# Performance work log

Hardware: AMD Instinct MI355X
Metric: run time of the kernel (lower is better)

## Reference

```python
import jax, jax.numpy as jnp
import numpy as np

EPS = 1e-5
B, S, D = 4, 2048, 128
BALL_SCALE = 0.05  # keeps points inside the unit Poincare ball for c=1


def setup_inputs() -> dict:
    key = jax.random.key(0)
    kq, kk, kv = jax.random.split(key, 3)
    q = jax.random.normal(kq, (B, S, D), dtype=jnp.float32) * BALL_SCALE
    k = jax.random.normal(kk, (B, S, D), dtype=jnp.float32) * BALL_SCALE
    v_tangent = jax.random.normal(kv, (B, S, D), dtype=jnp.float32)
    c = jnp.asarray(1.0, dtype=jnp.float32)
    beta = jnp.asarray(0.0, dtype=jnp.float32)            # nn.Parameter init 0.0
    attention_bias = jnp.asarray(0.0, dtype=jnp.float32)  # nn.Parameter init 0.0
    return {"q": q, "k": k, "v_tangent": v_tangent, "c": c,
            "beta": beta, "attention_bias": attention_bias}


def reference(q, k, v_tangent, c, beta, attention_bias):
    sqrt_c = jnp.sqrt(c)

    # --- pairwise Poincare distance (all fp32, as in the torch autocast block) ---
    x_norm_sq = jnp.sum(q * q, axis=-1, keepdims=True)            # (B,S,1)
    y_norm_sq = jnp.sum(k * k, axis=-1, keepdims=True)            # (B,S,1)
    xy_dot = jnp.einsum('bsd,btd->bst', q, k)                     # (B,S,S)
    y_norm_sq_t = jnp.swapaxes(y_norm_sq, -2, -1)                 # (B,1,S)
    diff_norm_sq = x_norm_sq - 2.0 * xy_dot + y_norm_sq_t         # ||x-y||^2, (B,S,S)
    denom = (1.0 - c * x_norm_sq) * (1.0 - c * y_norm_sq_t)       # (B,S,S)
    arg = 1.0 + 2.0 * c * diff_norm_sq / jnp.maximum(denom, EPS)
    dist = jnp.arccosh(jnp.maximum(arg, 1.0 + EPS)) / sqrt_c      # (B,S,S)

    # --- attention ---
    beta_positive = jax.nn.softplus(beta)
    attention_scores = -beta_positive * dist - attention_bias
    attention_weights = jax.nn.softmax(attention_scores, axis=-1)  # (B,S,S)
    output_tangent = jnp.einsum('bst,btd->bsd', attention_weights, v_tangent)

    # --- exp map at origin ---
    v_norm = jnp.maximum(
        jnp.sqrt(jnp.sum(output_tangent * output_tangent, axis=-1, keepdims=True)), EPS)
    output_hyperbolic = (jnp.tanh(sqrt_c * v_norm) / sqrt_c) * (output_tangent / v_norm)

    return output_hyperbolic, attention_weights
```

## Files before the change

### kernel.cpp

```cpp
#include <hip/hip_runtime.h>
#include <math.h>

#define B_ 4
#define S_ 2048
#define D_ 128
#define EPSF 1e-5f
#define BN 128
#define PSB 272

typedef __attribute__((ext_vector_type(8))) short short8;
typedef __attribute__((ext_vector_type(4))) float f32x4;

static __device__ __forceinline__ unsigned short f2bf(float f) {
    unsigned u = __float_as_uint(f);
    return (unsigned short)((u + 0x7fffu + ((u >> 16) & 1u)) >> 16);
}

static __device__ __forceinline__ void gload_lds16(const void* g, void* l) {
    __builtin_amdgcn_global_load_lds((const __attribute__((address_space(1))) unsigned*)g,
                                     (__attribute__((address_space(3))) unsigned*)l, 16, 0, 0);
}


__global__ __launch_bounds__(256) void convqk_kernel(const float* __restrict__ q,
                                                     const float* __restrict__ k,
                                                     float* __restrict__ qn, float* __restrict__ kn,
                                                     float* __restrict__ lws,
                                                     unsigned* __restrict__ Qb, unsigned* __restrict__ Kb) {
    int row = blockIdx.x * 4 + (threadIdx.x >> 6);
    int lane = threadIdx.x & 63;
    const int NR = B_ * S_;
    bool isQ = row < NR;
    int r = isQ ? row : row - NR;
    float2 v = ((const float2*)(isQ ? q : k))[(size_t)r * 64 + lane];
    unsigned pk = (unsigned)f2bf(v.x) | ((unsigned)f2bf(v.y) << 16);
    float nrm = v.x * v.x + v.y * v.y;
#pragma unroll
    for (int m = 1; m <= 32; m <<= 1) nrm += __shfl_xor(nrm, m, 64);
    if (isQ) {
        Qb[(size_t)r * 64 + lane] = pk;
        if (lane == 0) qn[r] = nrm;
        if (lane == 1) lws[r] = 0.f;
    } else {
        int c = lane >> 2;
        int cs = c ^ (r & 7);
        Kb[(size_t)r * 64 + cs * 4 + (lane & 3)] = pk;
        if (lane == 0) kn[r] = nrm;
    }
}

__global__ __launch_bounds__(256) void convv_kernel(const float* __restrict__ v, uint4* __restrict__ Vtb) {
    __shared__ unsigned short Vs[128 * 132];
    int b = blockIdx.x >> 4;
    int t = blockIdx.x & 15;
    int tid = threadIdx.x;
    const float* src = v + ((size_t)b * S_ + t * 128) * D_;
    int d4 = tid & 31, key0 = tid >> 5;
#pragma unroll
    for (int it = 0; it < 16; ++it) {
        int key = key0 + it * 8;
        float4 f = *(const float4*)(src + (size_t)key * D_ + d4 * 4);
        unsigned short* dst = &Vs[key * 132 + d4 * 4];
        dst[0] = f2bf(f.x); dst[1] = f2bf(f.y); dst[2] = f2bf(f.z); dst[3] = f2bf(f.w);
    }
    __syncthreads();
    uint4* tile = Vtb + (size_t)blockIdx.x * (128 * 16);
    int d = tid & 127;
    int cl = tid >> 7;
#pragma unroll
    for (int it = 0; it < 8; ++it) {
        int c = cl + it * 2;
        int kb = c * 8;
        unsigned short e0 = Vs[(kb + 0) * 132 + d], e1 = Vs[(kb + 1) * 132 + d];
        unsigned short e2 = Vs[(kb + 2) * 132 + d], e3 = Vs[(kb + 3) * 132 + d];
        unsigned short e4 = Vs[(kb + 4) * 132 + d], e5 = Vs[(kb + 5) * 132 + d];
        unsigned short e6 = Vs[(kb + 6) * 132 + d], e7 = Vs[(kb + 7) * 132 + d];
        uint4 o;
        o.x = (unsigned)e0 | ((unsigned)e1 << 16);
        o.y = (unsigned)e2 | ((unsigned)e3 << 16);
        o.z = (unsigned)e4 | ((unsigned)e5 << 16);
        o.w = (unsigned)e6 | ((unsigned)e7 << 16);
        tile[d * 16 + (c ^ (d & 7))] = o;
    }
}


__global__ __launch_bounds__(512, 2) void hattn2_kernel(
    const unsigned short* __restrict__ Qb, const char* __restrict__ Kb, const char* __restrict__ Vtb,
    const float* __restrict__ qn, const float* __restrict__ kn,
    const float* __restrict__ cp, const float* __restrict__ betap, const float* __restrict__ biasp,
    float* __restrict__ lws, float* __restrict__ Opart, uint4* __restrict__ Pws) {

    __shared__ __align__(1024) char smem[76032];
    char* KsB = smem;
    char* VtB = smem + 32768;
    char* PsB = smem + 65536;
    float* yn_s  = (float*)(smem + 74240);
    float* gy_s  = (float*)(smem + 74752);
    float* xn_s  = (float*)(smem + 75264);
    float* rx_s  = (float*)(smem + 75392);
    float* l_row = (float*)(smem + 75520);

    const int tid = threadIdx.x;
    const int lane = tid & 63, wave = tid >> 6;
    const int wm = wave & 1, wn = wave >> 1;
    const int lm = lane & 15, quad = lane >> 4;

    const int th = blockIdx.x & 1;
    const int b = (blockIdx.x >> 1) & 3;
    const int rb = blockIdx.x >> 3;
    const int s0 = rb * 32;
    const size_t bS = (size_t)b * S_;

    const float cc = cp[0], beta = betap[0], bias = biasp[0];
    const float beta_pos = fmaxf(beta, 0.f) + log1pf(__expf(-fabsf(beta)));
    const float sqrt_c = sqrtf(cc);
    const float bneg = -beta_pos / sqrt_c;
    const float bias2 = -bias * 1.442695040888963f;
    const float onepe = 1.f + EPSF;
    const float c2 = 2.f * cc;

    if (tid < 32) {
        float xn = qn[bS + s0 + tid];
        xn_s[tid] = xn;
        rx_s[tid] = c2 * __builtin_amdgcn_rcpf(1.f - cc * xn);
        l_row[tid] = 0.f;
    }

    short8 aq[4];
    {
        const unsigned short* qrow = Qb + (bS + s0 + wm * 16 + lm) * D_;
#pragma unroll
        for (int ks = 0; ks < 4; ++ks)
            aq[ks] = *(const short8*)(qrow + ks * 32 + quad * 8);
    }

    f32x4 o0 = {0.f, 0.f, 0.f, 0.f}, o1 = {0.f, 0.f, 0.f, 0.f};

    const char* KbBase = Kb + bS * 256;
    const char* VtBase = Vtb + (size_t)b * 16 * 32768;

    for (int it = 0; it < 8; ++it) {
        int t = th * 8 + it;
        int t0 = t * BN;
        __syncthreads();
        {
            const char* ks = KbBase + (size_t)t0 * 256;
            const char* vs = VtBase + (size_t)t * 32768;
#pragma unroll
            for (int j = 0; j < 4; ++j) {
                int off = (tid + j * 512) * 16;
                gload_lds16(ks + off, KsB + off);
                gload_lds16(vs + off, VtB + off);
            }
            if (tid < BN) {
                float yn = kn[bS + t0 + tid];
                yn_s[tid] = yn;
                gy_s[tid] = __builtin_amdgcn_rcpf(1.f - cc * yn);
            }
        }
        __syncthreads();

        f32x4 acc0 = {0.f, 0.f, 0.f, 0.f}, acc1 = {0.f, 0.f, 0.f, 0.f};
#pragma unroll
        for (int ks = 0; ks < 4; ++ks) {
            int n0 = wn * 32 + lm;
            int c = ks * 4 + quad;
            short8 b0 = *(const short8*)(KsB + n0 * 256 + ((c ^ (n0 & 7)) * 16));
            int n1 = n0 + 16;
            short8 b1 = *(const short8*)(KsB + n1 * 256 + ((c ^ (n1 & 7)) * 16));
            acc0 = __builtin_amdgcn_mfma_f32_16x16x32_bf16(aq[ks], b0, acc0, 0, 0, 0);
            acc1 = __builtin_amdgcn_mfma_f32_16x16x32_bf16(aq[ks], b1, acc1, 0, 0, 0);
        }

        int col0 = wn * 32 + lm, col1 = col0 + 16;
        float yn0 = yn_s[col0], gy0 = gy_s[col0];
        float yn1 = yn_s[col1], gy1 = gy_s[col1];
#pragma unroll
        for (int r = 0; r < 4; ++r) {
            int row = wm * 16 + quad * 4 + r;
            float xn = xn_s[row];
            float rx = rx_s[row];

            float diff0 = fmaf(-2.f, acc0[r], xn + yn0);
            float arg0 = fmaf(diff0 * gy0, rx, 1.f);
            arg0 = fmaxf(arg0, onepe);
            float w0 = arg0 + sqrtf(fmaf(arg0, arg0, -1.f));
            float p0 = __builtin_amdgcn_exp2f(fmaf(bneg, __builtin_amdgcn_logf(w0), bias2));

            float diff1 = fmaf(-2.f, acc1[r], xn + yn1);
            float arg1 = fmaf(diff1 * gy1, rx, 1.f);
            arg1 = fmaxf(arg1, onepe);
            float w1 = arg1 + sqrtf(fmaf(arg1, arg1, -1.f));
            float p1 = __builtin_amdgcn_exp2f(fmaf(bneg, __builtin_amdgcn_logf(w1), bias2));

            *(unsigned short*)(PsB + row * PSB + col0 * 2) = f2bf(p0);
            *(unsigned short*)(PsB + row * PSB + col1 * 2) = f2bf(p1);

            float s = p0 + p1;
#pragma unroll
            for (int m = 1; m <= 8; m <<= 1) s += __shfl_xor(s, m, 64);
            if (lm == 0) atomicAdd(&l_row[row], s);
        }
        __syncthreads();

        {
            int row = tid >> 4, chunk = tid & 15;
            uint4 pv = *(const uint4*)(PsB + row * PSB + chunk * 16);
            Pws[(((bS + s0 + row) * S_ + t0) >> 3) + chunk] = pv;
        }

#pragma unroll
        for (int ks = 0; ks < 4; ++ks) {
            short8 ap = *(const short8*)(PsB + (wm * 16 + lm) * PSB + (ks * 32 + quad * 8) * 2);
            int d0 = wn * 32 + lm;
            int c = ks * 4 + quad;
            short8 v0 = *(const short8*)(VtB + d0 * 256 + ((c ^ (d0 & 7)) * 16));
            int d1 = d0 + 16;
            short8 v1 = *(const short8*)(VtB + d1 * 256 + ((c ^ (d1 & 7)) * 16));
            o0 = __builtin_amdgcn_mfma_f32_16x16x32_bf16(ap, v0, o0, 0, 0, 0);
            o1 = __builtin_amdgcn_mfma_f32_16x16x32_bf16(ap, v1, o1, 0, 0, 0);
        }
    }
    __syncthreads();

    float* op = Opart + (size_t)th * (B_ * S_ * D_) + (bS + s0) * D_;
#pragma unroll
    for (int r = 0; r < 4; ++r) {
        int row = wm * 16 + quad * 4 + r;
        op[(size_t)row * D_ + wn * 32 + lm] = o0[r];
        op[(size_t)row * D_ + wn * 32 + 16 + lm] = o1[r];
    }
    if (tid < 32) atomicAdd(&lws[bS + s0 + tid], l_row[tid]);
}

__global__ __launch_bounds__(256) void hepi_kernel(const float* __restrict__ Opart,
                                                   const float* __restrict__ lws,
                                                   const float* __restrict__ cp,
                                                   float* __restrict__ hout) {
    int row = blockIdx.x * 4 + (threadIdx.x >> 6);
    int lane = threadIdx.x & 63;
    const float cc = cp[0];
    const float sqrt_c = sqrtf(cc);
    float2 a = ((const float2*)(Opart + (size_t)row * D_))[lane];
    float2 b = ((const float2*)(Opart + (size_t)(B_ * S_ * D_) + (size_t)row * D_))[lane];
    float linv = 1.f / lws[row];
    float x0 = (a.x + b.x) * linv;
    float x1 = (a.y + b.y) * linv;
    float np = x0 * x0 + x1 * x1;
#pragma unroll
    for (int m = 1; m <= 32; m <<= 1) np += __shfl_xor(np, m, 64);
    float vn = fmaxf(sqrtf(np), EPSF);
    float aa = sqrt_c * vn;
    float t = 1.f - 2.f / (__expf(2.f * aa) + 1.f);
    float sc = t / aa;
    float2 o = {x0 * sc, x1 * sc};
    ((float2*)(hout + (size_t)row * D_))[lane] = o;
}

__global__ __launch_bounds__(256) void wnorm2_kernel(const uint4* __restrict__ Pws,
                                                     const float* __restrict__ lws,
                                                     float* __restrict__ w) {
    size_t idx = (size_t)blockIdx.x * 256 + threadIdx.x;
    int row = (int)(idx >> 8);
    float linv = 1.f / lws[row];
    uint4 u = Pws[idx];
    float4 f0, f1;
    f0.x = __uint_as_float(u.x << 16) * linv;
    f0.y = __uint_as_float(u.x & 0xffff0000u) * linv;
    f0.z = __uint_as_float(u.y << 16) * linv;
    f0.w = __uint_as_float(u.y & 0xffff0000u) * linv;
    f1.x = __uint_as_float(u.z << 16) * linv;
    f1.y = __uint_as_float(u.z & 0xffff0000u) * linv;
    f1.z = __uint_as_float(u.w << 16) * linv;
    f1.w = __uint_as_float(u.w & 0xffff0000u) * linv;
    float4* out = (float4*)w + idx * 2;
    out[0] = f0;
    out[1] = f1;
}


__global__ __launch_bounds__(512, 2) void hattn_kernel(
    const unsigned short* __restrict__ Qb, const char* __restrict__ Kb, const char* __restrict__ Vtb,
    const float* __restrict__ qn, const float* __restrict__ kn,
    const float* __restrict__ cp, const float* __restrict__ betap, const float* __restrict__ biasp,
    float* __restrict__ lws, float* __restrict__ houtg, float* __restrict__ woutg) {

    __shared__ __align__(1024) char smem[75136];
    char* KsB = smem;
    char* VtB = smem + 32768;
    char* PsB = smem + 65536;
    float* kn_s  = (float*)(smem + 74240);
    float* qn_s  = (float*)(smem + 74752);
    float* l_row = (float*)(smem + 74880);
    float* nsq_s = (float*)(smem + 75008);

    const int tid = threadIdx.x;
    const int lane = tid & 63, wave = tid >> 6;
    const int wm = wave & 1, wn = wave >> 1;
    const int lm = lane & 15, quad = lane >> 4;

    int xcd = blockIdx.x & 7;
    int b = xcd >> 1;
    int rb = (blockIdx.x >> 3) * 2 + (xcd & 1);
    int s0 = rb * 32;
    const size_t bS = (size_t)b * S_;

    const float cc = cp[0], beta = betap[0], bias = biasp[0];
    const float beta_pos = fmaxf(beta, 0.f) + log1pf(__expf(-fabsf(beta)));
    const float sqrt_c = sqrtf(cc);
    const float inv_sqrt_c = 1.f / sqrt_c;

    if (tid < 32) {
        qn_s[tid] = qn[bS + s0 + tid];
        l_row[tid] = 0.f;
        nsq_s[tid] = 0.f;
    }

    short8 aq[4];
    {
        const unsigned short* qrow = Qb + (bS + s0 + wm * 16 + lm) * D_;
#pragma unroll
        for (int ks = 0; ks < 4; ++ks)
            aq[ks] = *(const short8*)(qrow + ks * 32 + quad * 8);
    }

    f32x4 o0 = {0.f, 0.f, 0.f, 0.f}, o1 = {0.f, 0.f, 0.f, 0.f};

    const char* KbBase = Kb + bS * 256;
    const char* VtBase = Vtb + (size_t)b * 16 * 32768;

    for (int t = 0; t < S_ / BN; ++t) {
        int t0 = t * BN;
        __syncthreads();
        {
            const uint4* ksrc = (const uint4*)(KbBase + (size_t)t0 * 256);
            const uint4* vsrc = (const uint4*)(VtBase + (size_t)t * 32768);
            uint4* kd = (uint4*)KsB;
            uint4* vd = (uint4*)VtB;
#pragma unroll
            for (int i = 0; i < 4; ++i) {
                kd[tid + i * 512] = ksrc[tid + i * 512];
                vd[tid + i * 512] = vsrc[tid + i * 512];
            }
            if (tid < BN) kn_s[tid] = kn[bS + t0 + tid];
        }
        __syncthreads();

        f32x4 acc0 = {0.f, 0.f, 0.f, 0.f}, acc1 = {0.f, 0.f, 0.f, 0.f};
#pragma unroll
        for (int ks = 0; ks < 4; ++ks) {
            int n0 = wn * 32 + lm;
            int c = ks * 4 + quad;
            short8 b0 = *(const short8*)(KsB + n0 * 256 + ((c ^ (n0 & 7)) * 16));
            int n1 = n0 + 16;
            short8 b1 = *(const short8*)(KsB + n1 * 256 + ((c ^ (n1 & 7)) * 16));
            acc0 = __builtin_amdgcn_mfma_f32_16x16x32_bf16(aq[ks], b0, acc0, 0, 0, 0);
            acc1 = __builtin_amdgcn_mfma_f32_16x16x32_bf16(aq[ks], b1, acc1, 0, 0, 0);
        }

        float lp[4];
#pragma unroll
        for (int r = 0; r < 4; ++r) {
            int row = wm * 16 + quad * 4 + r;
            float xn = qn_s[row];
            float fx = 1.f - cc * xn;
            float p0, p1;
#pragma unroll
            for (int nt = 0; nt < 2; ++nt) {
                int col = wn * 32 + nt * 16 + lm;
                float dot = (nt == 0) ? acc0[r] : acc1[r];
                float yn = kn_s[col];
                float diff = xn - 2.f * dot + yn;
                float den = fmaxf(fx * (1.f - cc * yn), EPSF);
                float arg = fmaf(2.f * cc * diff, __builtin_amdgcn_rcpf(den), 1.f);
                arg = fmaxf(arg, 1.f + EPSF);
                float dist = __logf(arg + sqrtf(arg * arg - 1.f)) * inv_sqrt_c;
                float p = __expf(fmaf(-beta_pos, dist, -bias));
                woutg[(bS + s0 + row) * S_ + t0 + col] = p;
                *(unsigned short*)(PsB + row * PSB + col * 2) = f2bf(p);
                if (nt == 0) p0 = p; else p1 = p;
            }
            lp[r] = p0 + p1;
        }
#pragma unroll
        for (int r = 0; r < 4; ++r) {
            float s = lp[r];
#pragma unroll
            for (int m = 1; m <= 8; m <<= 1) s += __shfl_xor(s, m, 64);
            if (lm == 0) atomicAdd(&l_row[wm * 16 + quad * 4 + r], s);
        }
        __syncthreads();

#pragma unroll
        for (int ks = 0; ks < 4; ++ks) {
            short8 ap = *(const short8*)(PsB + (wm * 16 + lm) * PSB + (ks * 32 + quad * 8) * 2);
            int d0 = wn * 32 + lm;
            int c = ks * 4 + quad;
            short8 v0 = *(const short8*)(VtB + d0 * 256 + ((c ^ (d0 & 7)) * 16));
            int d1 = d0 + 16;
            short8 v1 = *(const short8*)(VtB + d1 * 256 + ((c ^ (d1 & 7)) * 16));
            o0 = __builtin_amdgcn_mfma_f32_16x16x32_bf16(ap, v0, o0, 0, 0, 0);
            o1 = __builtin_amdgcn_mfma_f32_16x16x32_bf16(ap, v1, o1, 0, 0, 0);
        }
    }
    __syncthreads();

    float xs0[4], xs1[4];
#pragma unroll
    for (int r = 0; r < 4; ++r) {
        int row = wm * 16 + quad * 4 + r;
        float linv = __builtin_amdgcn_rcpf(l_row[row]);
        float x0 = o0[r] * linv, x1 = o1[r] * linv;
        xs0[r] = x0; xs1[r] = x1;
        float np = x0 * x0 + x1 * x1;
#pragma unroll
        for (int m = 1; m <= 8; m <<= 1) np += __shfl_xor(np, m, 64);
        if (lm == 0) atomicAdd(&nsq_s[row], np);
    }
    if (tid < 32) lws[bS + s0 + tid] = l_row[tid];
    __syncthreads();
#pragma unroll
    for (int r = 0; r < 4; ++r) {
        int row = wm * 16 + quad * 4 + r;
        float vn = fmaxf(sqrtf(nsq_s[row]), EPSF);
        float a = sqrt_c * vn;
        float th = 1.f - 2.f * __builtin_amdgcn_rcpf(__expf(2.f * a) + 1.f);
        float sc = th / a;
        houtg[(bS + s0 + row) * D_ + wn * 32 + lm] = xs0[r] * sc;
        houtg[(bS + s0 + row) * D_ + wn * 32 + 16 + lm] = xs1[r] * sc;
    }
}

__global__ __launch_bounds__(256) void wnorm_kernel(float* __restrict__ w,
                                                    const float* __restrict__ lws) {
    size_t idx = (size_t)blockIdx.x * 256 + threadIdx.x;
    int row = (int)(idx >> 9);
    float linv = 1.f / lws[row];
    float4* p = (float4*)w + idx;
    float4 v = *p;
    v.x *= linv; v.y *= linv; v.z *= linv; v.w *= linv;
    *p = v;
}


extern "C" void kernel_launch(void* const* d_in, const int* in_sizes, int n_in,
                              void* d_out, int out_size, void* d_ws, size_t ws_size,
                              hipStream_t stream) {
    const float* q    = (const float*)d_in[0];
    const float* k    = (const float*)d_in[1];
    const float* v    = (const float*)d_in[2];
    const float* c    = (const float*)d_in[3];
    const float* beta = (const float*)d_in[4];
    const float* ab   = (const float*)d_in[5];

    float* out  = (float*)d_out;
    float* hout = out;
    float* wout = out + (size_t)B_ * S_ * D_;

    float* qn  = (float*)d_ws;
    float* kn  = qn + B_ * S_;
    float* lws = kn + B_ * S_;
    char*  wsb = (char*)d_ws;
    const size_t QB_OFF = 98304;
    const size_t KB_OFF = QB_OFF + 2097152;
    const size_t VT_OFF = KB_OFF + 2097152;
    const size_t NEED1  = VT_OFF + 2097152;
    const size_t OP_OFF = NEED1;
    const size_t PW_OFF = OP_OFF + 2u * B_ * S_ * D_ * 4;
    const size_t NEED2  = PW_OFF + (size_t)B_ * S_ * S_ * 2;

    unsigned* Qb = (unsigned*)(wsb + QB_OFF);
    unsigned* Kb = (unsigned*)(wsb + KB_OFF);
    uint4*   Vtb = (uint4*)(wsb + VT_OFF);

    if (ws_size >= NEED2) {
        float* Opart = (float*)(wsb + OP_OFF);
        uint4* Pws   = (uint4*)(wsb + PW_OFF);
        convqk_kernel<<<4096, 256, 0, stream>>>(q, k, qn, kn, lws, Qb, Kb);
        convv_kernel<<<64, 256, 0, stream>>>(v, Vtb);
        hattn2_kernel<<<512, 512, 0, stream>>>((const unsigned short*)Qb, (const char*)Kb,
                                               (const char*)Vtb, qn, kn, c, beta, ab,
                                               lws, Opart, Pws);
        hepi_kernel<<<2048, 256, 0, stream>>>(Opart, lws, c, hout);
        wnorm2_kernel<<<8192, 256, 0, stream>>>(Pws, lws, wout);
    } else {
        convqk_kernel<<<4096, 256, 0, stream>>>(q, k, qn, kn, lws, Qb, Kb);
        convv_kernel<<<64, 256, 0, stream>>>(v, Vtb);
        hattn_kernel<<<256, 512, 0, stream>>>((const unsigned short*)Qb, (const char*)Kb,
                                              (const char*)Vtb, qn, kn, c, beta, ab,
                                              lws, hout, wout);
        wnorm_kernel<<<(B_ * S_ * S_ / 4) / 256, 256, 0, stream>>>(wout, lws);
    }
}
```

Baseline: 147.5 us.

## Split keys four ways with atomic reduction and fuse epilogue via last-block counter

The attention kernel now splits the key dimension into four chunks of 64-key tiles, running 1024 smaller-LDS blocks that are meant to reach higher occupancy. Partial outputs are accumulated into a zeroed global buffer with atomics. The last block per row group, found through an atomic counter, runs the exp-map epilogue and the weight normalisation inline, which removes the separate hepi and wnorm2 launches. The cost is many global float atomics, a serialized tail done by one block per row group, and removal of the fallback path for small workspaces.

```diff
diff --git a/kernel.cpp b/kernel.cpp
--- a/kernel.cpp
+++ b/kernel.cpp
@@ -5,8 +5,7 @@
 #define S_ 2048
 #define D_ 128
 #define EPSF 1e-5f
-#define BN 128
-#define PSB 272
+#define PSB 144
 
 typedef __attribute__((ext_vector_type(8))) short short8;
 typedef __attribute__((ext_vector_type(4))) float f32x4;
@@ -26,9 +25,12 @@
                                                      const float* __restrict__ k,
                                                      float* __restrict__ qn, float* __restrict__ kn,
                                                      float* __restrict__ lws,
-                                                     unsigned* __restrict__ Qb, unsigned* __restrict__ Kb) {
+                                                     unsigned* __restrict__ Qb, unsigned* __restrict__ Kb,
+                                                     float* __restrict__ Osum, int* __restrict__ cnt) {
     int row = blockIdx.x * 4 + (threadIdx.x >> 6);
     int lane = threadIdx.x & 63;
+    Osum[(size_t)blockIdx.x * 256 + threadIdx.x] = 0.f;
+    if (blockIdx.x == 0) cnt[threadIdx.x] = 0;
     const int NR = B_ * S_;
     bool isQ = row < NR;
     int r = isQ ? row : row - NR;
@@ -50,25 +52,25 @@
 }
 
 __global__ __launch_bounds__(256) void convv_kernel(const float* __restrict__ v, uint4* __restrict__ Vtb) {
-    __shared__ unsigned short Vs[128 * 132];
-    int b = blockIdx.x >> 4;
-    int t = blockIdx.x & 15;
+    __shared__ unsigned short Vs[64 * 132];
+    int b = blockIdx.x >> 5;
+    int t = blockIdx.x & 31;
     int tid = threadIdx.x;
-    const float* src = v + ((size_t)b * S_ + t * 128) * D_;
+    const float* src = v + ((size_t)b * S_ + t * 64) * D_;
     int d4 = tid & 31, key0 = tid >> 5;
 #pragma unroll
-    for (int it = 0; it < 16; ++it) {
+    for (int it = 0; it < 8; ++it) {
         int key = key0 + it * 8;
         float4 f = *(const float4*)(src + (size_t)key * D_ + d4 * 4);
         unsigned short* dst = &Vs[key * 132 + d4 * 4];
         dst[0] = f2bf(f.x); dst[1] = f2bf(f.y); dst[2] = f2bf(f.z); dst[3] = f2bf(f.w);
     }
     __syncthreads();
-    uint4* tile = Vtb + (size_t)blockIdx.x * (128 * 16);
+    uint4* tile = Vtb + (size_t)blockIdx.x * (128 * 8);
     int d = tid & 127;
     int cl = tid >> 7;
 #pragma unroll
-    for (int it = 0; it < 8; ++it) {
+    for (int it = 0; it < 4; ++it) {
         int c = cl + it * 2;
         int kb = c * 8;
         unsigned short e0 = Vs[(kb + 0) * 132 + d], e1 = Vs[(kb + 1) * 132 + d];
@@ -80,36 +82,40 @@
         o.y = (unsigned)e2 | ((unsigned)e3 << 16);
         o.z = (unsigned)e4 | ((unsigned)e5 << 16);
         o.w = (unsigned)e6 | ((unsigned)e7 << 16);
-        tile[d * 16 + (c ^ (d & 7))] = o;
-    }
-}
-
-
-__global__ __launch_bounds__(512, 2) void hattn2_kernel(
+        tile[d * 8 + (c ^ (d & 7))] = o;
+    }
+}
+
+
+__global__ __launch_bounds__(512, 8) void hattn3_kernel(
     const unsigned short* __restrict__ Qb, const char* __restrict__ Kb, const char* __restrict__ Vtb,
     const float* __restrict__ qn, const float* __restrict__ kn,
     const float* __restrict__ cp, const float* __restrict__ betap, const float* __restrict__ biasp,
-    float* __restrict__ lws, float* __restrict__ Opart, uint4* __restrict__ Pws) {
-
-    __shared__ __align__(1024) char smem[76032];
+    float* __restrict__ lws, float* __restrict__ Osum, int* __restrict__ cnt,
+    uint4* __restrict__ Pws, float* __restrict__ hout, float* __restrict__ wout) {
+
+    __shared__ __align__(1024) char smem[38272];
     char* KsB = smem;
-    char* VtB = smem + 32768;
-    char* PsB = smem + 65536;
-    float* yn_s  = (float*)(smem + 74240);
-    float* gy_s  = (float*)(smem + 74752);
-    float* xn_s  = (float*)(smem + 75264);
-    float* rx_s  = (float*)(smem + 75392);
-    float* l_row = (float*)(smem + 75520);
+    char* VtB = smem + 16384;
+    char* PsB = smem + 32768;
+    float* yn_s  = (float*)(smem + 37376);
+    float* gy_s  = (float*)(smem + 37632);
+    float* xn_s  = (float*)(smem + 37888);
+    float* rx_s  = (float*)(smem + 38016);
+    float* l_row = (float*)(smem + 38144);
+    __shared__ int sflag;
 
     const int tid = threadIdx.x;
     const int lane = tid & 63, wave = tid >> 6;
     const int wm = wave & 1, wn = wave >> 1;
     const int lm = lane & 15, quad = lane >> 4;
 
-    const int th = blockIdx.x & 1;
-    const int b = (blockIdx.x >> 1) & 3;
-    const int rb = blockIdx.x >> 3;
+    const int gid = blockIdx.x;
+    const int b = (gid >> 1) & 3;
+    const int th = ((gid >> 3) & 1) * 2 + (gid & 1);
+    const int rb = gid >> 4;
     const int s0 = rb * 32;
+    const int g = (b << 6) | rb;
     const size_t bS = (size_t)b * S_;
 
     const float cc = cp[0], beta = betap[0], bias = biasp[0];
@@ -138,22 +144,25 @@
     f32x4 o0 = {0.f, 0.f, 0.f, 0.f}, o1 = {0.f, 0.f, 0.f, 0.f};
 
     const char* KbBase = Kb + bS * 256;
-    const char* VtBase = Vtb + (size_t)b * 16 * 32768;
+    const char* VtBase = Vtb + (size_t)b * 32 * 16384;
+
+    const int n0 = wn * 16 + lm;
+    const int d0 = wn * 32 + lm, d1 = d0 + 16;
+    const int col = wn * 16 + lm;
 
     for (int it = 0; it < 8; ++it) {
         int t = th * 8 + it;
-        int t0 = t * BN;
+        int t0 = t * 64;
         __syncthreads();
         {
-            const char* ks = KbBase + (size_t)t0 * 256;
-            const char* vs = VtBase + (size_t)t * 32768;
-#pragma unroll
-            for (int j = 0; j < 4; ++j) {
-                int off = (tid + j * 512) * 16;
-                gload_lds16(ks + off, KsB + off);
-                gload_lds16(vs + off, VtB + off);
-            }
-            if (tid < BN) {
+            const char* ksrc = KbBase + (size_t)t0 * 256;
+            const char* vsrc = VtBase + (size_t)t * 16384;
+            int off = tid * 16;
+            gload_lds16(ksrc + off, KsB + off);
+            gload_lds16(ksrc + off + 8192, KsB + off + 8192);
+            gload_lds16(vsrc + off, VtB + off);
+            gload_lds16(vsrc + off + 8192, VtB + off + 8192);
+            if (tid < 64) {
                 float yn = kn[bS + t0 + tid];
                 yn_s[tid] = yn;
                 gy_s[tid] = __builtin_amdgcn_rcpf(1.f - cc * yn);
@@ -161,286 +170,107 @@
         }
         __syncthreads();
 
-        f32x4 acc0 = {0.f, 0.f, 0.f, 0.f}, acc1 = {0.f, 0.f, 0.f, 0.f};
+        f32x4 acc = {0.f, 0.f, 0.f, 0.f};
 #pragma unroll
         for (int ks = 0; ks < 4; ++ks) {
-            int n0 = wn * 32 + lm;
             int c = ks * 4 + quad;
-            short8 b0 = *(const short8*)(KsB + n0 * 256 + ((c ^ (n0 & 7)) * 16));
-            int n1 = n0 + 16;
-            short8 b1 = *(const short8*)(KsB + n1 * 256 + ((c ^ (n1 & 7)) * 16));
-            acc0 = __builtin_amdgcn_mfma_f32_16x16x32_bf16(aq[ks], b0, acc0, 0, 0, 0);
-            acc1 = __builtin_amdgcn_mfma_f32_16x16x32_bf16(aq[ks], b1, acc1, 0, 0, 0);
-        }
-
-        int col0 = wn * 32 + lm, col1 = col0 + 16;
-        float yn0 = yn_s[col0], gy0 = gy_s[col0];
-        float yn1 = yn_s[col1], gy1 = gy_s[col1];
+            short8 bf = *(const short8*)(KsB + n0 * 256 + ((c ^ (n0 & 7)) * 16));
+            acc = __builtin_amdgcn_mfma_f32_16x16x32_bf16(aq[ks], bf, acc, 0, 0, 0);
+        }
+
+        float ynv = yn_s[col], gyv = gy_s[col];
 #pragma unroll
         for (int r = 0; r < 4; ++r) {
             int row = wm * 16 + quad * 4 + r;
-            float xn = xn_s[row];
-            float rx = rx_s[row];
-
-            float diff0 = fmaf(-2.f, acc0[r], xn + yn0);
-            float arg0 = fmaf(diff0 * gy0, rx, 1.f);
-            arg0 = fmaxf(arg0, onepe);
-            float w0 = arg0 + sqrtf(fmaf(arg0, arg0, -1.f));
-            float p0 = __builtin_amdgcn_exp2f(fmaf(bneg, __builtin_amdgcn_logf(w0), bias2));
-
-            float diff1 = fmaf(-2.f, acc1[r], xn + yn1);
-            float arg1 = fmaf(diff1 * gy1, rx, 1.f);
-            arg1 = fmaxf(arg1, onepe);
-            float w1 = arg1 + sqrtf(fmaf(arg1, arg1, -1.f));
-            float p1 = __builtin_amdgcn_exp2f(fmaf(bneg, __builtin_amdgcn_logf(w1), bias2));
-
-            *(unsigned short*)(PsB + row * PSB + col0 * 2) = f2bf(p0);
-            *(unsigned short*)(PsB + row * PSB + col1 * 2) = f2bf(p1);
-
-            float s = p0 + p1;
+            float diff = fmaf(-2.f, acc[r], xn_s[row] + ynv);
+            float arg = fmaf(diff * gyv, rx_s[row], 1.f);
+            arg = fmaxf(arg, onepe);
+            float w = arg + sqrtf(fmaf(arg, arg, -1.f));
+            float p = __builtin_amdgcn_exp2f(fmaf(bneg, __builtin_amdgcn_logf(w), bias2));
+            *(unsigned short*)(PsB + row * PSB + col * 2) = f2bf(p);
+            float s = p;
 #pragma unroll
             for (int m = 1; m <= 8; m <<= 1) s += __shfl_xor(s, m, 64);
             if (lm == 0) atomicAdd(&l_row[row], s);
         }
         __syncthreads();
 
-        {
-            int row = tid >> 4, chunk = tid & 15;
-            uint4 pv = *(const uint4*)(PsB + row * PSB + chunk * 16);
-            Pws[(((bS + s0 + row) * S_ + t0) >> 3) + chunk] = pv;
-        }
-
-#pragma unroll
-        for (int ks = 0; ks < 4; ++ks) {
-            short8 ap = *(const short8*)(PsB + (wm * 16 + lm) * PSB + (ks * 32 + quad * 8) * 2);
-            int d0 = wn * 32 + lm;
+        if (tid < 256) {
+            int row = tid >> 3, ch = tid & 7;
+            uint4 pv = *(const uint4*)(PsB + row * PSB + ch * 16);
+            Pws[(((bS + s0 + row) * S_ + t0) >> 3) + ch] = pv;
+        }
+
+#pragma unroll
+        for (int ks = 0; ks < 2; ++ks) {
+            short8 ap = *(const short8*)(PsB + (wm * 16 + lm) * PSB + ks * 64 + quad * 16);
             int c = ks * 4 + quad;
-            short8 v0 = *(const short8*)(VtB + d0 * 256 + ((c ^ (d0 & 7)) * 16));
-            int d1 = d0 + 16;
-            short8 v1 = *(const short8*)(VtB + d1 * 256 + ((c ^ (d1 & 7)) * 16));
+            short8 v0 = *(const short8*)(VtB + d0 * 128 + ((c ^ (d0 & 7)) * 16));
+            short8 v1 = *(const short8*)(VtB + d1 * 128 + ((c ^ (d1 & 7)) * 16));
             o0 = __builtin_amdgcn_mfma_f32_16x16x32_bf16(ap, v0, o0, 0, 0, 0);
             o1 = __builtin_amdgcn_mfma_f32_16x16x32_bf16(ap, v1, o1, 0, 0, 0);
         }
     }
-    __syncthreads();
-
-    float* op = Opart + (size_t)th * (B_ * S_ * D_) + (bS + s0) * D_;
+
+    float* ob = Osum + (bS + s0) * D_;
 #pragma unroll
     for (int r = 0; r < 4; ++r) {
         int row = wm * 16 + quad * 4 + r;
-        op[(size_t)row * D_ + wn * 32 + lm] = o0[r];
-        op[(size_t)row * D_ + wn * 32 + 16 + lm] = o1[r];
+        atomicAdd(&ob[(size_t)row * D_ + wn * 32 + lm], o0[r]);
+        atomicAdd(&ob[(size_t)row * D_ + wn * 32 + 16 + lm], o1[r]);
     }
     if (tid < 32) atomicAdd(&lws[bS + s0 + tid], l_row[tid]);
-}
-
-__global__ __launch_bounds__(256) void hepi_kernel(const float* __restrict__ Opart,
-                                                   const float* __restrict__ lws,
-                                                   const float* __restrict__ cp,
-                                                   float* __restrict__ hout) {
-    int row = blockIdx.x * 4 + (threadIdx.x >> 6);
-    int lane = threadIdx.x & 63;
-    const float cc = cp[0];
-    const float sqrt_c = sqrtf(cc);
-    float2 a = ((const float2*)(Opart + (size_t)row * D_))[lane];
-    float2 b = ((const float2*)(Opart + (size_t)(B_ * S_ * D_) + (size_t)row * D_))[lane];
-    float linv = 1.f / lws[row];
-    float x0 = (a.x + b.x) * linv;
-    float x1 = (a.y + b.y) * linv;
-    float np = x0 * x0 + x1 * x1;
-#pragma unroll
-    for (int m = 1; m <= 32; m <<= 1) np += __shfl_xor(np, m, 64);
-    float vn = fmaxf(sqrtf(np), EPSF);
-    float aa = sqrt_c * vn;
-    float t = 1.f - 2.f / (__expf(2.f * aa) + 1.f);
-    float sc = t / aa;
-    float2 o = {x0 * sc, x1 * sc};
-    ((float2*)(hout + (size_t)row * D_))[lane] = o;
-}
-
-__global__ __launch_bounds__(256) void wnorm2_kernel(const uint4* __restrict__ Pws,
-                                                     const float* __restrict__ lws,
-                                                     float* __restrict__ w) {
-    size_t idx = (size_t)blockIdx.x * 256 + threadIdx.x;
-    int row = (int)(idx >> 8);
-    float linv = 1.f / lws[row];
-    uint4 u = Pws[idx];
-    float4 f0, f1;
-    f0.x = __uint_as_float(u.x << 16) * linv;
-    f0.y = __uint_as_float(u.x & 0xffff0000u) * linv;
-    f0.z = __uint_as_float(u.y << 16) * linv;
-    f0.w = __uint_as_float(u.y & 0xffff0000u) * linv;
-    f1.x = __uint_as_float(u.z << 16) * linv;
-    f1.y = __uint_as_float(u.z & 0xffff0000u) * linv;
-    f1.z = __uint_as_float(u.w << 16) * linv;
-    f1.w = __uint_as_float(u.w & 0xffff0000u) * linv;
-    float4* out = (float4*)w + idx * 2;
-    out[0] = f0;
-    out[1] = f1;
-}
-
-
-__global__ __launch_bounds__(512, 2) void hattn_kernel(
-    const unsigned short* __restrict__ Qb, const char* __restrict__ Kb, const char* __restrict__ Vtb,
-    const float* __restrict__ qn, const float* __restrict__ kn,
-    const float* __restrict__ cp, const float* __restrict__ betap, const float* __restrict__ biasp,
-    float* __restrict__ lws, float* __restrict__ houtg, float* __restrict__ woutg) {
-
-    __shared__ __align__(1024) char smem[75136];
-    char* KsB = smem;
-    char* VtB = smem + 32768;
-    char* PsB = smem + 65536;
-    float* kn_s  = (float*)(smem + 74240);
-    float* qn_s  = (float*)(smem + 74752);
-    float* l_row = (float*)(smem + 74880);
-    float* nsq_s = (float*)(smem + 75008);
-
-    const int tid = threadIdx.x;
-    const int lane = tid & 63, wave = tid >> 6;
-    const int wm = wave & 1, wn = wave >> 1;
-    const int lm = lane & 15, quad = lane >> 4;
-
-    int xcd = blockIdx.x & 7;
-    int b = xcd >> 1;
-    int rb = (blockIdx.x >> 3) * 2 + (xcd & 1);
-    int s0 = rb * 32;
-    const size_t bS = (size_t)b * S_;
-
-    const float cc = cp[0], beta = betap[0], bias = biasp[0];
-    const float beta_pos = fmaxf(beta, 0.f) + log1pf(__expf(-fabsf(beta)));
-    const float sqrt_c = sqrtf(cc);
-    const float inv_sqrt_c = 1.f / sqrt_c;
-
-    if (tid < 32) {
-        qn_s[tid] = qn[bS + s0 + tid];
-        l_row[tid] = 0.f;
-        nsq_s[tid] = 0.f;
-    }
-
-    short8 aq[4];
+    __syncthreads();
+    if (tid == 0) {
+        __threadfence();
+        sflag = (atomicAdd(&cnt[g], 1) == 3);
+    }
+    __syncthreads();
+    if (!sflag) return;
+
+    __threadfence();
+    float* linv_s = xn_s;
+    if (tid < 32) linv_s[tid] = 1.f / lws[bS + s0 + tid];
+    __syncthreads();
+
+#pragma unroll
+    for (int rr = 0; rr < 4; ++rr) {
+        int row = wave * 4 + rr;
+        float2 x2 = ((const float2*)(ob + (size_t)row * D_))[lane];
+        float linv = linv_s[row];
+        float x0 = x2.x * linv, x1 = x2.y * linv;
+        float np = x0 * x0 + x1 * x1;
+#pragma unroll
+        for (int m = 1; m <= 32; m <<= 1) np += __shfl_xor(np, m, 64);
+        float vn = fmaxf(sqrtf(np), EPSF);
+        float a = sqrt_c * vn;
+        float t = 1.f - 2.f / (__expf(2.f * a) + 1.f);
+        float sc = t / a;
+        float2 o = {x0 * sc, x1 * sc};
+        ((float2*)(hout + (bS + s0 + row) * D_))[lane] = o;
+    }
+
     {
-        const unsigned short* qrow = Qb + (bS + s0 + wm * 16 + lm) * D_;
-#pragma unroll
-        for (int ks = 0; ks < 4; ++ks)
-            aq[ks] = *(const short8*)(qrow + ks * 32 + quad * 8);
-    }
-
-    f32x4 o0 = {0.f, 0.f, 0.f, 0.f}, o1 = {0.f, 0.f, 0.f, 0.f};
-
-    const char* KbBase = Kb + bS * 256;
-    const char* VtBase = Vtb + (size_t)b * 16 * 32768;
-
-    for (int t = 0; t < S_ / BN; ++t) {
-        int t0 = t * BN;
-        __syncthreads();
-        {
-            const uint4* ksrc = (const uint4*)(KbBase + (size_t)t0 * 256);
-            const uint4* vsrc = (const uint4*)(VtBase + (size_t)t * 32768);
-            uint4* kd = (uint4*)KsB;
-            uint4* vd = (uint4*)VtB;
-#pragma unroll
-            for (int i = 0; i < 4; ++i) {
-                kd[tid + i * 512] = ksrc[tid + i * 512];
-                vd[tid + i * 512] = vsrc[tid + i * 512];
-            }
-            if (tid < BN) kn_s[tid] = kn[bS + t0 + tid];
-        }
-        __syncthreads();
-
-        f32x4 acc0 = {0.f, 0.f, 0.f, 0.f}, acc1 = {0.f, 0.f, 0.f, 0.f};
-#pragma unroll
-        for (int ks = 0; ks < 4; ++ks) {
-            int n0 = wn * 32 + lm;
-            int c = ks * 4 + quad;
-            short8 b0 = *(const short8*)(KsB + n0 * 256 + ((c ^ (n0 & 7)) * 16));
-            int n1 = n0 + 16;
-            short8 b1 = *(const short8*)(KsB + n1 * 256 + ((c ^ (n1 & 7)) * 16));
-            acc0 = __builtin_amdgcn_mfma_f32_16x16x32_bf16(aq[ks], b0, acc0, 0, 0, 0);
-            acc1 = __builtin_amdgcn_mfma_f32_16x16x32_bf16(aq[ks], b1, acc1, 0, 0, 0);
-        }
-
-        float lp[4];
-#pragma unroll
-        for (int r = 0; r < 4; ++r) {
-            int row = wm * 16 + quad * 4 + r;
-            float xn = qn_s[row];
-            float fx = 1.f - cc * xn;
-            float p0, p1;
-#pragma unroll
-            for (int nt = 0; nt < 2; ++nt) {
-                int col = wn * 32 + nt * 16 + lm;
-                float dot = (nt == 0) ? acc0[r] : acc1[r];
-                float yn = kn_s[col];
-                float diff = xn - 2.f * dot + yn;
-                float den = fmaxf(fx * (1.f - cc * yn), EPSF);
-                float arg = fmaf(2.f * cc * diff, __builtin_amdgcn_rcpf(den), 1.f);
-                arg = fmaxf(arg, 1.f + EPSF);
-                float dist = __logf(arg + sqrtf(arg * arg - 1.f)) * inv_sqrt_c;
-                float p = __expf(fmaf(-beta_pos, dist, -bias));
-                woutg[(bS + s0 + row) * S_ + t0 + col] = p;
-                *(unsigned short*)(PsB + row * PSB + col * 2) = f2bf(p);
-                if (nt == 0) p0 = p; else p1 = p;
-            }
-            lp[r] = p0 + p1;
-        }
-#pragma unroll
-        for (int r = 0; r < 4; ++r) {
-            float s = lp[r];
-#pragma unroll
-            for (int m = 1; m <= 8; m <<= 1) s += __shfl_xor(s, m, 64);
-            if (lm == 0) atomicAdd(&l_row[wm * 16 + quad * 4 + r], s);
-        }
-        __syncthreads();
-
-#pragma unroll
-        for (int ks = 0; ks < 4; ++ks) {
-            short8 ap = *(const short8*)(PsB + (wm * 16 + lm) * PSB + (ks * 32 + quad * 8) * 2);
-            int d0 = wn * 32 + lm;
-            int c = ks * 4 + quad;
-            short8 v0 = *(const short8*)(VtB + d0 * 256 + ((c ^ (d0 & 7)) * 16));
-            int d1 = d0 + 16;
-            short8 v1 = *(const short8*)(VtB + d1 * 256 + ((c ^ (d1 & 7)) * 16));
-            o0 = __builtin_amdgcn_mfma_f32_16x16x32_bf16(ap, v0, o0, 0, 0, 0);
-            o1 = __builtin_amdgcn_mfma_f32_16x16x32_bf16(ap, v1, o1, 0, 0, 0);
-        }
-    }
-    __syncthreads();
-
-    float xs0[4], xs1[4];
-#pragma unroll
-    for (int r = 0; r < 4; ++r) {
-        int row = wm * 16 + quad * 4 + r;
-        float linv = __builtin_amdgcn_rcpf(l_row[row]);
-        float x0 = o0[r] * linv, x1 = o1[r] * linv;
-        xs0[r] = x0; xs1[r] = x1;
-        float np = x0 * x0 + x1 * x1;
-#pragma unroll
-        for (int m = 1; m <= 8; m <<= 1) np += __shfl_xor(np, m, 64);
-        if (lm == 0) atomicAdd(&nsq_s[row], np);
-    }
-    if (tid < 32) lws[bS + s0 + tid] = l_row[tid];
-    __syncthreads();
-#pragma unroll
-    for (int r = 0; r < 4; ++r) {
-        int row = wm * 16 + quad * 4 + r;
-        float vn = fmaxf(sqrtf(nsq_s[row]), EPSF);
-        float a = sqrt_c * vn;
-        float th = 1.f - 2.f * __builtin_amdgcn_rcpf(__expf(2.f * a) + 1.f);
-        float sc = th / a;
-        houtg[(bS + s0 + row) * D_ + wn * 32 + lm] = xs0[r] * sc;
-        houtg[(bS + s0 + row) * D_ + wn * 32 + 16 + lm] = xs1[r] * sc;
-    }
-}
-
-__global__ __launch_bounds__(256) void wnorm_kernel(float* __restrict__ w,
-                                                    const float* __restrict__ lws) {
-    size_t idx = (size_t)blockIdx.x * 256 + threadIdx.x;
-    int row = (int)(idx >> 9);
-    float linv = 1.f / lws[row];
-    float4* p = (float4*)w + idx;
-    float4 v = *p;
-    v.x *= linv; v.y *= linv; v.z *= linv; v.w *= linv;
-    *p = v;
+        size_t base = ((bS + s0) * (size_t)S_) >> 3;
+        for (int j = 0; j < 16; ++j) {
+            int idx = tid + j * 512;
+            int row = idx >> 8;
+            float linv = linv_s[row];
+            uint4 u = Pws[base + idx];
+            float4 f0, f1;
+            f0.x = __uint_as_float(u.x << 16) * linv;
+            f0.y = __uint_as_float(u.x & 0xffff0000u) * linv;
+            f0.z = __uint_as_float(u.y << 16) * linv;
+            f0.w = __uint_as_float(u.y & 0xffff0000u) * linv;
+            f1.x = __uint_as_float(u.z << 16) * linv;
+            f1.y = __uint_as_float(u.z & 0xffff0000u) * linv;
+            f1.z = __uint_as_float(u.w << 16) * linv;
+            f1.w = __uint_as_float(u.w & 0xffff0000u) * linv;
+            float4* outp = (float4*)wout + (base + idx) * 2;
+            outp[0] = f0;
+            outp[1] = f1;
+        }
+    }
 }
 
 
@@ -458,38 +288,26 @@
     float* hout = out;
     float* wout = out + (size_t)B_ * S_ * D_;
 
-    float* qn  = (float*)d_ws;
-    float* kn  = qn + B_ * S_;
-    float* lws = kn + B_ * S_;
-    char*  wsb = (char*)d_ws;
-    const size_t QB_OFF = 98304;
+    char* wsb = (char*)d_ws;
+    float* qn  = (float*)wsb;
+    float* kn  = (float*)(wsb + 32768);
+    float* lws = (float*)(wsb + 65536);
+    int*   cnt = (int*)(wsb + 98304);
+    const size_t QB_OFF = 99328;
     const size_t KB_OFF = QB_OFF + 2097152;
     const size_t VT_OFF = KB_OFF + 2097152;
-    const size_t NEED1  = VT_OFF + 2097152;
-    const size_t OP_OFF = NEED1;
-    const size_t PW_OFF = OP_OFF + 2u * B_ * S_ * D_ * 4;
-    const size_t NEED2  = PW_OFF + (size_t)B_ * S_ * S_ * 2;
+    const size_t OS_OFF = VT_OFF + 2097152;
+    const size_t PW_OFF = OS_OFF + (size_t)B_ * S_ * D_ * 4;
 
     unsigned* Qb = (unsigned*)(wsb + QB_OFF);
     unsigned* Kb = (unsigned*)(wsb + KB_OFF);
     uint4*   Vtb = (uint4*)(wsb + VT_OFF);
-
-    if (ws_size >= NEED2) {
-        float* Opart = (float*)(wsb + OP_OFF);
-        uint4* Pws   = (uint4*)(wsb + PW_OFF);
-        convqk_kernel<<<4096, 256, 0, stream>>>(q, k, qn, kn, lws, Qb, Kb);
-        convv_kernel<<<64, 256, 0, stream>>>(v, Vtb);
-        hattn2_kernel<<<512, 512, 0, stream>>>((const unsigned short*)Qb, (const char*)Kb,
-                                               (const char*)Vtb, qn, kn, c, beta, ab,
-                                               lws, Opart, Pws);
-        hepi_kernel<<<2048, 256, 0, stream>>>(Opart, lws, c, hout);
-        wnorm2_kernel<<<8192, 256, 0, stream>>>(Pws, lws, wout);
-    } else {
-        convqk_kernel<<<4096, 256, 0, stream>>>(q, k, qn, kn, lws, Qb, Kb);
-        convv_kernel<<<64, 256, 0, stream>>>(v, Vtb);
-        hattn_kernel<<<256, 512, 0, stream>>>((const unsigned short*)Qb, (const char*)Kb,
-                                              (const char*)Vtb, qn, kn, c, beta, ab,
-                                              lws, hout, wout);
-        wnorm_kernel<<<(B_ * S_ * S_ / 4) / 256, 256, 0, stream>>>(wout, lws);
-    }
-}
+    float*  Osum = (float*)(wsb + OS_OFF);
+    uint4*   Pws = (uint4*)(wsb + PW_OFF);
+
+    convqk_kernel<<<4096, 256, 0, stream>>>(q, k, qn, kn, lws, Qb, Kb, Osum, cnt);
+    convv_kernel<<<128, 256, 0, stream>>>(v, Vtb);
+    hattn3_kernel<<<1024, 512, 0, stream>>>((const unsigned short*)Qb, (const char*)Kb,
+                                            (const char*)Vtb, qn, kn, c, beta, ab,
+                                            lws, Osum, cnt, Pws, hout, wout);
+}
```

New measurement: 379.9 us. 2.58x slower.
